# Kernel tuning notes

Hardware: AMD Instinct MI355X
Metric: run time of the kernel (lower is better)

The kernel has to match this reference:

```python
import jax, jax.numpy as jnp
import numpy as np


def lsigf_db(h, S, x, b):
    """Time-varying delayed graph filter (LSIGF_DB).
    h: (F, E, K, G) filter taps; S: (B, T, E, N, N) batch time-varying GSO;
    x: (B, T, G, N) node signals; b: (F, 1) bias or None.
    Diffusion recursion: x_k(t) = x_{k-1}(t-1) @ S(t)  (zero signal before t=0).
    """
    K = h.shape[2]
    B, T, E, N, _ = S.shape
    G = x.shape[2]
    xk = jnp.broadcast_to(x[:, :, None], (B, T, E, G, N))  # k = 0 tap
    zs = [xk]
    for _ in range(1, K):
        # delay one time step: x(t-1), zero-padded at t=0
        xk = jnp.concatenate([jnp.zeros_like(xk[:, :1]), xk[:, :-1]], axis=1)
        # shift by current GSO: matmul(x, S) as in the torch implementation
        xk = jnp.einsum('btegm,btemn->btegn', xk, S)
        zs.append(xk)
    z = jnp.stack(zs, axis=2)  # (B, T, K, E, G, N)
    y = jnp.einsum('fekg,btkegn->btfn', h, z)  # (B, T, F, N)
    if b is not None:
        y = y + b[None, None]  # (F,1) broadcasts over nodes
    return y


def setup_inputs() -> dict:
    key = jax.random.key(0)
    ks = jax.random.split(key, 12)
    B, T, E, N = 8, 64, 1, 256
    F0, F1, F2 = 12, 64, 32
    K1, K2 = 3, 3
    R1, R2 = 32, 2

    def u(k, shape, fan):
        s = 1.0 / np.sqrt(fan)
        return jax.random.uniform(k, shape, jnp.float32, -s, s)

    return {
        'x': jax.random.normal(ks[0], (B, T, F0, N), jnp.float32),
        'S': jax.random.normal(ks[1], (B, T, E, N, N), jnp.float32),
        'W1': u(ks[2], (F1, E, K1, F0), F0 * K1),
        'b1': u(ks[3], (F1, 1), F0 * K1),
        'W2': u(ks[4], (F2, E, K2, F1), F1 * K2),
        'b2': u(ks[5], (F2, 1), F1 * K2),
        'A1': u(ks[6], (R1, F2), F2),
        'c1': u(ks[7], (R1,), F2),
        'A2': u(ks[8], (R2, R1), R1),
        'c2': u(ks[9], (R2,), R1),
    }


def reference(x, S, W1, b1, W2, b2, A1, c1, A2, c2):
    # Graph filtering layers (GraphFilter_DB + Tanh)
    y = jnp.tanh(lsigf_db(W1, S, x, b1))
    y = jnp.tanh(lsigf_db(W2, S, y, b2))
    # Local readout: per-node MLP Linear -> Tanh -> Linear
    y = jnp.swapaxes(y, 2, 3)  # (B, T, N, F2)
    y = jnp.tanh(y @ A1.T + c1)
    y = y @ A2.T + c2
    return jnp.swapaxes(y, 2, 3)  # (B, T, dimReadout[-1], N)
```

## Files before the change

### kernel.cpp

```cpp
#include <hip/hip_runtime.h>
#include <hip/hip_fp16.h>

typedef _Float16 half8 __attribute__((ext_vector_type(8)));
typedef _Float16 half4v __attribute__((ext_vector_type(4)));
typedef float f32x4 __attribute__((ext_vector_type(4)));

static constexpr int B_ = 8, T_ = 64, N_ = 256;
static constexpr int F0 = 12, F1 = 64, F2 = 32;
static constexpr int BT_ = B_ * T_;

__device__ inline float tanh_fast(float x) {
    x = fminf(20.f, fmaxf(-20.f, x));
    float e = __expf(2.f * x);
    return (e - 1.f) / (e + 1.f);
}

__global__ __launch_bounds__(512) void k_transpose_s(const float* __restrict__ S,
                              _Float16* __restrict__ STh, _Float16* __restrict__ STl) {
    __shared__ float tile[64][129];
    int bt = blockIdx.x;
    int n0 = blockIdx.y * 64;
    const float* s = S + (size_t)bt * N_ * N_;
    _Float16* sth = STh + (size_t)bt * N_ * N_;
    _Float16* stl = STl + (size_t)bt * N_ * N_;
    int q = threadIdx.x & 15;
    int r0 = threadIdx.x >> 4;
    int q2 = threadIdx.x & 7;
    int nr = threadIdx.x >> 3;
    for (int m0 = 0; m0 < N_; m0 += 128) {
        #pragma unroll
        for (int rr = r0; rr < 128; rr += 32) {
            f32x4 v = __builtin_nontemporal_load(
                (const f32x4*)(s + (size_t)(m0 + rr) * N_ + n0 + q * 4));
            tile[q * 4 + 0][rr] = v[0];
            tile[q * 4 + 1][rr] = v[1];
            tile[q * 4 + 2][rr] = v[2];
            tile[q * 4 + 3][rr] = v[3];
        }
        __syncthreads();
        #pragma unroll
        for (int ci = 0; ci < 2; ++ci) {
            int mc = ci * 8 + q2;
            half8 h, l;
            #pragma unroll
            for (int e = 0; e < 8; ++e) {
                float v = tile[nr][mc * 8 + e];
                _Float16 hh = (_Float16)v;
                h[e] = hh;
                l[e] = (_Float16)(v - (float)hh);
            }
            size_t o = (size_t)(n0 + nr) * N_ + m0 + mc * 8;
            *(half8*)(sth + o) = h;
            *(half8*)(stl + o) = l;
        }
        __syncthreads();
    }
}

__global__ void k_transpose_x(const float* __restrict__ x,
                              _Float16* __restrict__ XTh, _Float16* __restrict__ XTl) {
    int bt = blockIdx.x;
    int n = threadIdx.x;
    const float* xc = x + (size_t)bt * F0 * N_;
    half8 hb[2] = {}, lb[2] = {};
    #pragma unroll
    for (int g = 0; g < F0; ++g) {
        float v = xc[(size_t)g * N_ + n];
        _Float16 hh = (_Float16)v;
        hb[g >> 3][g & 7] = hh;
        lb[g >> 3][g & 7] = (_Float16)(v - (float)hh);
    }
    size_t o = ((size_t)bt * N_ + n) * 16;
    *(half8*)(XTh + o) = hb[0];
    *(half8*)(XTh + o + 8) = hb[1];
    *(half8*)(XTl + o) = lb[0];
    *(half8*)(XTl + o + 8) = lb[1];
}

__global__ void k_chain1x(const float* __restrict__ x,
                          const _Float16* __restrict__ STh, const _Float16* __restrict__ STl,
                          _Float16* __restrict__ Oh, _Float16* __restrict__ Ol,
                          _Float16* __restrict__ OTh, _Float16* __restrict__ OTl) {
    int bt = blockIdx.x;
    int t = bt & (T_ - 1);
    int wave = threadIdx.x >> 6;
    int lane = threadIdx.x & 63;
    int l15 = lane & 15;
    int lk = lane >> 4;
    int n0 = blockIdx.y * 128 + wave * 32;

    f32x4 acc[2];
    #pragma unroll
    for (int j = 0; j < 2; ++j) acc[j] = (f32x4){0.f, 0.f, 0.f, 0.f};

    if (t > 0) {
        const float* A = x + (size_t)(bt - 1) * F0 * N_;
        const _Float16* B_h = STh + (size_t)bt * N_ * N_;
        const _Float16* B_l = STl + (size_t)bt * N_ * N_;
        #pragma unroll
        for (int kk = 0; kk < 8; ++kk) {
            int kof = kk * 32 + lk * 8;
            half8 ah = {}, al = {};
            if (l15 < F0) {
                const float* ar = A + (size_t)l15 * N_ + kof;
                float4 v0 = *(const float4*)(ar);
                float4 v1 = *(const float4*)(ar + 4);
                float vv[8] = {v0.x, v0.y, v0.z, v0.w, v1.x, v1.y, v1.z, v1.w};
                #pragma unroll
                for (int c = 0; c < 8; ++c) {
                    _Float16 hh = (_Float16)vv[c];
                    ah[c] = hh;
                    al[c] = (_Float16)(vv[c] - (float)hh);
                }
            }
            #pragma unroll
            for (int j = 0; j < 2; ++j) {
                half8 bh = *(const half8*)(B_h + (size_t)(n0 + j * 16 + l15) * N_ + kof);
                half8 bl = *(const half8*)(B_l + (size_t)(n0 + j * 16 + l15) * N_ + kof);
                acc[j] = __builtin_amdgcn_mfma_f32_16x16x32_f16(ah, bh, acc[j], 0, 0, 0);
                acc[j] = __builtin_amdgcn_mfma_f32_16x16x32_f16(al, bh, acc[j], 0, 0, 0);
                acc[j] = __builtin_amdgcn_mfma_f32_16x16x32_f16(ah, bl, acc[j], 0, 0, 0);
            }
        }
    }
    _Float16* O_h = Oh + (size_t)bt * 16 * N_;
    _Float16* O_l = Ol + (size_t)bt * 16 * N_;
    #pragma unroll
    for (int j = 0; j < 2; ++j) {
        half4v th, tl;
        #pragma unroll
        for (int r = 0; r < 4; ++r) {
            float v = acc[j][r];
            _Float16 h = (_Float16)v;
            size_t idx = (size_t)(lk * 4 + r) * N_ + n0 + j * 16 + l15;
            O_h[idx] = h;
            O_l[idx] = (_Float16)(v - (float)h);
            th[r] = h;
            tl[r] = (_Float16)(v - (float)h);
        }
        size_t to = ((size_t)bt * N_ + n0 + j * 16 + l15) * 16 + lk * 4;
        *(half4v*)(OTh + to) = th;
        *(half4v*)(OTl + to) = tl;
    }
}

__global__ void k_chainV1(const _Float16* __restrict__ Ah, const _Float16* __restrict__ Al,
                          const _Float16* __restrict__ STh, const _Float16* __restrict__ STl,
                          _Float16* __restrict__ OTh, _Float16* __restrict__ OTl) {
    int bt = blockIdx.x;
    int t = bt & (T_ - 1);
    int wave = threadIdx.x >> 6;
    int lane = threadIdx.x & 63;
    int l15 = lane & 15;
    int lk = lane >> 4;
    int n0 = blockIdx.y * 128 + wave * 32;

    f32x4 acc[2];
    #pragma unroll
    for (int j = 0; j < 2; ++j) acc[j] = (f32x4){0.f, 0.f, 0.f, 0.f};

    if (t > 0) {
        const _Float16* A_h = Ah + (size_t)(bt - 1) * 16 * N_;
        const _Float16* A_l = Al + (size_t)(bt - 1) * 16 * N_;
        const _Float16* B_h = STh + (size_t)bt * N_ * N_;
        const _Float16* B_l = STl + (size_t)bt * N_ * N_;
        #pragma unroll
        for (int kk = 0; kk < 8; ++kk) {
            int kof = kk * 32 + lk * 8;
            half8 ah = *(const half8*)(A_h + (size_t)l15 * N_ + kof);
            half8 al = *(const half8*)(A_l + (size_t)l15 * N_ + kof);
            #pragma unroll
            for (int j = 0; j < 2; ++j) {
                half8 bh = *(const half8*)(B_h + (size_t)(n0 + j * 16 + l15) * N_ + kof);
                half8 bl = *(const half8*)(B_l + (size_t)(n0 + j * 16 + l15) * N_ + kof);
                acc[j] = __builtin_amdgcn_mfma_f32_16x16x32_f16(ah, bh, acc[j], 0, 0, 0);
                acc[j] = __builtin_amdgcn_mfma_f32_16x16x32_f16(al, bh, acc[j], 0, 0, 0);
                acc[j] = __builtin_amdgcn_mfma_f32_16x16x32_f16(ah, bl, acc[j], 0, 0, 0);
            }
        }
    }
    #pragma unroll
    for (int j = 0; j < 2; ++j) {
        half4v th, tl;
        #pragma unroll
        for (int r = 0; r < 4; ++r) {
            float v = acc[j][r];
            _Float16 h = (_Float16)v;
            th[r] = h;
            tl[r] = (_Float16)(v - (float)h);
        }
        size_t to = ((size_t)bt * N_ + n0 + j * 16 + l15) * 16 + lk * 4;
        *(half4v*)(OTh + to) = th;
        *(half4v*)(OTl + to) = tl;
    }
}

__global__ void k_combine1(const _Float16* __restrict__ XTh, const _Float16* __restrict__ XTl,
                           const _Float16* __restrict__ U1Th, const _Float16* __restrict__ U1Tl,
                           const _Float16* __restrict__ V1Th, const _Float16* __restrict__ V1Tl,
                           const float* __restrict__ W1, const float* __restrict__ b1,
                           _Float16* __restrict__ Y1Th, _Float16* __restrict__ Y1Tl) {
    __shared__ _Float16 wh[64 * 72], wl[64 * 72];
    int bt = blockIdx.x;
    int tid = threadIdx.x;
    for (int i = tid; i < 64 * 72; i += 256) {
        int f = i / 72, k = i % 72;
        float v = 0.f;
        if (k < 12) v = W1[f * 36 + k];
        else if (k >= 16 && k < 28) v = W1[f * 36 + 12 + (k - 16)];
        else if (k >= 32 && k < 44) v = W1[f * 36 + 24 + (k - 32)];
        _Float16 hh = (_Float16)v;
        wh[i] = hh;
        wl[i] = (_Float16)(v - (float)hh);
    }
    __syncthreads();

    int wv = tid >> 6, lane = tid & 63, l15 = lane & 15, lk = lane >> 4;
    int n0 = wv * 64;
    f32x4 acc[4][4];
    #pragma unroll
    for (int i = 0; i < 4; ++i)
        #pragma unroll
        for (int j = 0; j < 4; ++j) acc[i][j] = (f32x4){0.f, 0.f, 0.f, 0.f};

    #pragma unroll
    for (int kk = 0; kk < 2; ++kk) {
        half8 bh[4], bl[4];
        #pragma unroll
        for (int j = 0; j < 4; ++j) {
            size_t base16 = ((size_t)bt * N_ + n0 + j * 16 + l15) * 16;
            if (kk == 0) {
                if (lk < 2) {
                    bh[j] = *(const half8*)(XTh + base16 + lk * 8);
                    bl[j] = *(const half8*)(XTl + base16 + lk * 8);
                } else {
                    bh[j] = *(const half8*)(U1Th + base16 + (lk - 2) * 8);
                    bl[j] = *(const half8*)(U1Tl + base16 + (lk - 2) * 8);
                }
            } else {
                if (lk < 2) {
                    bh[j] = *(const half8*)(V1Th + base16 + lk * 8);
                    bl[j] = *(const half8*)(V1Tl + base16 + lk * 8);
                } else {
                    bh[j] = half8{};
                    bl[j] = half8{};
                }
            }
        }
        #pragma unroll
        for (int i = 0; i < 4; ++i) {
            half8 ah = *(const half8*)(wh + (i * 16 + l15) * 72 + kk * 32 + lk * 8);
            half8 al = *(const half8*)(wl + (i * 16 + l15) * 72 + kk * 32 + lk * 8);
            #pragma unroll
            for (int j = 0; j < 4; ++j) {
                acc[i][j] = __builtin_amdgcn_mfma_f32_16x16x32_f16(ah, bh[j], acc[i][j], 0, 0, 0);
                acc[i][j] = __builtin_amdgcn_mfma_f32_16x16x32_f16(al, bh[j], acc[i][j], 0, 0, 0);
                acc[i][j] = __builtin_amdgcn_mfma_f32_16x16x32_f16(ah, bl[j], acc[i][j], 0, 0, 0);
            }
        }
    }
    #pragma unroll
    for (int i = 0; i < 4; ++i) {
        float bb[4];
        #pragma unroll
        for (int r = 0; r < 4; ++r) bb[r] = b1[i * 16 + lk * 4 + r];
        #pragma unroll
        for (int j = 0; j < 4; ++j) {
            half4v th, tl;
            #pragma unroll
            for (int r = 0; r < 4; ++r) {
                float yv = tanh_fast(acc[i][j][r] + bb[r]);
                _Float16 h = (_Float16)yv;
                th[r] = h;
                tl[r] = (_Float16)(yv - (float)h);
            }
            size_t to = ((size_t)bt * N_ + n0 + j * 16 + l15) * 64 + i * 16 + lk * 4;
            *(half4v*)(Y1Th + to) = th;
            *(half4v*)(Y1Tl + to) = tl;
        }
    }
}

__global__ void k_proj(const _Float16* __restrict__ Y1Th, const _Float16* __restrict__ Y1Tl,
                       const float* __restrict__ W2,
                       _Float16* __restrict__ Gh, _Float16* __restrict__ Gl,
                       float* __restrict__ Hf, float* __restrict__ Y2a) {
    __shared__ _Float16 wh[96 * 72], wl[96 * 72];
    int bt = blockIdx.x;
    int tid = threadIdx.x;
    for (int i = tid; i < 96 * 64; i += 256) {
        int r = i >> 6, g = i & 63;
        int f, off;
        if (r < 32)      { f = r;      off = 128; }
        else if (r < 64) { f = r - 32; off = 64;  }
        else             { f = r - 64; off = 0;   }
        float v = W2[f * 192 + off + g];
        _Float16 hh = (_Float16)v;
        wh[r * 72 + g] = hh;
        wl[r * 72 + g] = (_Float16)(v - (float)hh);
    }
    __syncthreads();

    int wv = tid >> 6, lane = tid & 63, l15 = lane & 15, lk = lane >> 4;
    int n0 = wv * 64;
    f32x4 acc[6][4];
    #pragma unroll
    for (int i = 0; i < 6; ++i)
        #pragma unroll
        for (int j = 0; j < 4; ++j) acc[i][j] = (f32x4){0.f, 0.f, 0.f, 0.f};

    const _Float16* Bh = Y1Th + (size_t)bt * N_ * 64;
    const _Float16* Bl = Y1Tl + (size_t)bt * N_ * 64;
    #pragma unroll
    for (int kk = 0; kk < 2; ++kk) {
        int kof = kk * 32 + lk * 8;
        half8 bh[4], bl[4];
        #pragma unroll
        for (int j = 0; j < 4; ++j) {
            bh[j] = *(const half8*)(Bh + (size_t)(n0 + j * 16 + l15) * 64 + kof);
            bl[j] = *(const half8*)(Bl + (size_t)(n0 + j * 16 + l15) * 64 + kof);
        }
        #pragma unroll
        for (int i = 0; i < 6; ++i) {
            half8 ah = *(const half8*)(wh + (i * 16 + l15) * 72 + kof);
            half8 al = *(const half8*)(wl + (i * 16 + l15) * 72 + kof);
            #pragma unroll
            for (int j = 0; j < 4; ++j) {
                acc[i][j] = __builtin_amdgcn_mfma_f32_16x16x32_f16(ah, bh[j], acc[i][j], 0, 0, 0);
                acc[i][j] = __builtin_amdgcn_mfma_f32_16x16x32_f16(al, bh[j], acc[i][j], 0, 0, 0);
                acc[i][j] = __builtin_amdgcn_mfma_f32_16x16x32_f16(ah, bl[j], acc[i][j], 0, 0, 0);
            }
        }
    }
    #pragma unroll
    for (int i = 0; i < 6; ++i)
        #pragma unroll
        for (int j = 0; j < 4; ++j)
            #pragma unroll
            for (int r = 0; r < 4; ++r) {
                int row = i * 16 + lk * 4 + r;
                int col = n0 + j * 16 + l15;
                float v = acc[i][j][r];
                if (row < 32) {
                    _Float16 hh = (_Float16)v;
                    size_t o = ((size_t)bt * 32 + row) * N_ + col;
                    Gh[o] = hh;
                    Gl[o] = (_Float16)(v - (float)hh);
                } else if (row < 64) {
                    Hf[((size_t)bt * 32 + row - 32) * N_ + col] = v;
                } else {
                    Y2a[((size_t)bt * 32 + row - 64) * N_ + col] = v;
                }
            }
}

__global__ void k_chainR(const _Float16* __restrict__ Gh, const _Float16* __restrict__ Gl,
                         const _Float16* __restrict__ STh, const _Float16* __restrict__ STl,
                         const float* __restrict__ Hf,
                         _Float16* __restrict__ Rh, _Float16* __restrict__ Rl) {
    int bt = blockIdx.x;
    int t = bt & (T_ - 1);
    int wave = threadIdx.x >> 6;
    int lane = threadIdx.x & 63;
    int l15 = lane & 15;
    int lk = lane >> 4;
    int n0 = blockIdx.y * 128 + wave * 32;

    f32x4 acc[2][2];
    #pragma unroll
    for (int i = 0; i < 2; ++i)
        #pragma unroll
        for (int j = 0; j < 2; ++j) acc[i][j] = (f32x4){0.f, 0.f, 0.f, 0.f};

    if (t > 0) {
        const _Float16* A_h = Gh + (size_t)(bt - 1) * 32 * N_;
        const _Float16* A_l = Gl + (size_t)(bt - 1) * 32 * N_;
        const _Float16* B_h = STh + (size_t)bt * N_ * N_;
        const _Float16* B_l = STl + (size_t)bt * N_ * N_;
        #pragma unroll
        for (int kk = 0; kk < 8; ++kk) {
            int kof = kk * 32 + lk * 8;
            half8 ah[2], al[2];
            #pragma unroll
            for (int i = 0; i < 2; ++i) {
                ah[i] = *(const half8*)(A_h + (size_t)(i * 16 + l15) * N_ + kof);
                al[i] = *(const half8*)(A_l + (size_t)(i * 16 + l15) * N_ + kof);
            }
            #pragma unroll
            for (int j = 0; j < 2; ++j) {
                half8 bh = *(const half8*)(B_h + (size_t)(n0 + j * 16 + l15) * N_ + kof);
                half8 bl = *(const half8*)(B_l + (size_t)(n0 + j * 16 + l15) * N_ + kof);
                #pragma unroll
                for (int i = 0; i < 2; ++i) {
                    acc[i][j] = __builtin_amdgcn_mfma_f32_16x16x32_f16(ah[i], bh, acc[i][j], 0, 0, 0);
                    acc[i][j] = __builtin_amdgcn_mfma_f32_16x16x32_f16(al[i], bh, acc[i][j], 0, 0, 0);
                    acc[i][j] = __builtin_amdgcn_mfma_f32_16x16x32_f16(ah[i], bl, acc[i][j], 0, 0, 0);
                }
            }
        }
    }
    const float* Hb = Hf + (size_t)bt * 32 * N_;
    _Float16* R_h = Rh + (size_t)bt * 32 * N_;
    _Float16* R_l = Rl + (size_t)bt * 32 * N_;
    #pragma unroll
    for (int i = 0; i < 2; ++i)
        #pragma unroll
        for (int j = 0; j < 2; ++j)
            #pragma unroll
            for (int r = 0; r < 4; ++r) {
                size_t idx = (size_t)(i * 16 + lk * 4 + r) * N_ + n0 + j * 16 + l15;
                float v = acc[i][j][r] + Hb[idx];
                _Float16 h = (_Float16)v;
                R_h[idx] = h;
                R_l[idx] = (_Float16)(v - (float)h);
            }
}

__global__ void k_chainY2(const _Float16* __restrict__ Rh, const _Float16* __restrict__ Rl,
                          const _Float16* __restrict__ STh, const _Float16* __restrict__ STl,
                          const float* __restrict__ Y2a, const float* __restrict__ b2,
                          const float* __restrict__ A1, const float* __restrict__ c1,
                          const float* __restrict__ A2, const float* __restrict__ c2,
                          float* __restrict__ out) {
    __shared__ float y2s[32 * 133];
    __shared__ float la1[32 * 33];
    int bt = blockIdx.x;
    int t = bt & (T_ - 1);
    int tid = threadIdx.x;
    for (int i = tid; i < 32 * 32; i += 256) la1[(i >> 5) * 33 + (i & 31)] = A1[i];

    int wave = tid >> 6;
    int lane = tid & 63;
    int l15 = lane & 15;
    int lk = lane >> 4;
    int n0 = blockIdx.y * 128 + wave * 32;

    f32x4 acc[2][2];
    #pragma unroll
    for (int i = 0; i < 2; ++i)
        #pragma unroll
        for (int j = 0; j < 2; ++j) acc[i][j] = (f32x4){0.f, 0.f, 0.f, 0.f};

    if (t > 0) {
        const _Float16* A_h = Rh + (size_t)(bt - 1) * 32 * N_;
        const _Float16* A_l = Rl + (size_t)(bt - 1) * 32 * N_;
        const _Float16* B_h = STh + (size_t)bt * N_ * N_;
        const _Float16* B_l = STl + (size_t)bt * N_ * N_;
        #pragma unroll
        for (int kk = 0; kk < 8; ++kk) {
            int kof = kk * 32 + lk * 8;
            half8 ah[2], al[2];
            #pragma unroll
            for (int i = 0; i < 2; ++i) {
                ah[i] = *(const half8*)(A_h + (size_t)(i * 16 + l15) * N_ + kof);
                al[i] = *(const half8*)(A_l + (size_t)(i * 16 + l15) * N_ + kof);
            }
            #pragma unroll
            for (int j = 0; j < 2; ++j) {
                half8 bh = *(const half8*)(B_h + (size_t)(n0 + j * 16 + l15) * N_ + kof);
                half8 bl = *(const half8*)(B_l + (size_t)(n0 + j * 16 + l15) * N_ + kof);
                #pragma unroll
                for (int i = 0; i < 2; ++i) {
                    acc[i][j] = __builtin_amdgcn_mfma_f32_16x16x32_f16(ah[i], bh, acc[i][j], 0, 0, 0);
                    acc[i][j] = __builtin_amdgcn_mfma_f32_16x16x32_f16(al[i], bh, acc[i][j], 0, 0, 0);
                    acc[i][j] = __builtin_amdgcn_mfma_f32_16x16x32_f16(ah[i], bl, acc[i][j], 0, 0, 0);
                }
            }
        }
    }
    const float* Ya = Y2a + (size_t)bt * 32 * N_;
    int colb0 = wave * 32;
    #pragma unroll
    for (int i = 0; i < 2; ++i)
        #pragma unroll
        for (int j = 0; j < 2; ++j)
            #pragma unroll
            for (int r = 0; r < 4; ++r) {
                int row = i * 16 + lk * 4 + r;
                int colb = colb0 + j * 16 + l15;
                int n = blockIdx.y * 128 + colb;
                y2s[row * 133 + colb] = acc[i][j][r] + Ya[(size_t)row * N_ + n] + b2[row];
            }
    __syncthreads();

    if (tid < 128) {
        int colb = tid;
        int n = blockIdx.y * 128 + colb;
        float y2v[32];
        #pragma unroll
        for (int f = 0; f < 32; ++f) y2v[f] = tanh_fast(y2s[f * 133 + colb]);
        float o0 = 0.f, o1 = 0.f;
        #pragma unroll
        for (int j = 0; j < 32; ++j) {
            const float* a1r = la1 + j * 33;
            float s = c1[j];
            #pragma unroll
            for (int f = 0; f < 32; ++f) s += a1r[f] * y2v[f];
            float hj = tanh_fast(s);
            o0 += A2[j] * hj;
            o1 += A2[32 + j] * hj;
        }
        out[((size_t)bt * 2 + 0) * N_ + n] = o0 + c2[0];
        out[((size_t)bt * 2 + 1) * N_ + n] = o1 + c2[1];
    }
}

extern "C" void kernel_launch(void* const* d_in, const int* in_sizes, int n_in,
                              void* d_out, int out_size, void* d_ws, size_t ws_size,
                              hipStream_t stream) {
    const float* x  = (const float*)d_in[0];
    const float* S  = (const float*)d_in[1];
    const float* W1 = (const float*)d_in[2];
    const float* b1 = (const float*)d_in[3];
    const float* W2 = (const float*)d_in[4];
    const float* b2 = (const float*)d_in[5];
    const float* A1 = (const float*)d_in[6];
    const float* c1 = (const float*)d_in[7];
    const float* A2 = (const float*)d_in[8];
    const float* c2 = (const float*)d_in[9];
    float* out = (float*)d_out;

    char* ws = (char*)d_ws;
    const size_t SZ_ST  = (size_t)BT_ * N_ * N_ * 2;
    const size_t SZ_Y1T = (size_t)BT_ * N_ * 64 * 2;
    const size_t SZ_G   = (size_t)BT_ * 32 * N_ * 2;
    const size_t SZ_H   = (size_t)BT_ * 32 * N_ * 4;
    const size_t SZ_T16 = (size_t)BT_ * N_ * 16 * 2;
    size_t off = 0;
    _Float16* STh  = (_Float16*)(ws + off); off += SZ_ST;
    _Float16* STl  = (_Float16*)(ws + off); off += SZ_ST;
    _Float16* Y1Th = (_Float16*)(ws + off); off += SZ_Y1T;
    _Float16* Y1Tl = (_Float16*)(ws + off); off += SZ_Y1T;
    _Float16* Gh   = (_Float16*)(ws + off); off += SZ_G;
    _Float16* Gl   = (_Float16*)(ws + off); off += SZ_G;
    float*    Hf   = (float*)(ws + off); off += SZ_H;
    float*    Y2a  = (float*)(ws + off); off += SZ_H;
    _Float16* Rh   = (_Float16*)(ws + off); off += SZ_G;
    _Float16* Rl   = (_Float16*)(ws + off); off += SZ_G;
    if (ws_size < off) return;

    _Float16* XTh  = (_Float16*)Hf;
    _Float16* XTl  = XTh + SZ_T16 / 2;
    _Float16* U1Th = (_Float16*)Y2a;
    _Float16* U1Tl = U1Th + SZ_T16 / 2;
    _Float16* V1Th = U1Tl + SZ_T16 / 2;
    _Float16* V1Tl = V1Th + SZ_T16 / 2;
    _Float16* U1h  = Rh;
    _Float16* U1l  = Rl;

    k_transpose_s<<<dim3(BT_, 4), 512, 0, stream>>>(S, STh, STl);
    k_transpose_x<<<BT_, 256, 0, stream>>>(x, XTh, XTl);
    k_chain1x<<<dim3(BT_, 2), 256, 0, stream>>>(x, STh, STl, U1h, U1l, U1Th, U1Tl);
    k_chainV1<<<dim3(BT_, 2), 256, 0, stream>>>(U1h, U1l, STh, STl, V1Th, V1Tl);
    k_combine1<<<BT_, 256, 0, stream>>>(XTh, XTl, U1Th, U1Tl, V1Th, V1Tl, W1, b1, Y1Th, Y1Tl);
    k_proj<<<BT_, 256, 0, stream>>>(Y1Th, Y1Tl, W2, Gh, Gl, Hf, Y2a);
    k_chainR<<<dim3(BT_, 2), 256, 0, stream>>>(Gh, Gl, STh, STl, Hf, Rh, Rl);
    k_chainY2<<<dim3(BT_, 2), 256, 0, stream>>>(Rh, Rl, STh, STl, Y2a, b2,
                                                A1, c1, A2, c2, out);
}
```

Measured before the change: 247.4 us.

## Fuse first diffusion step into S transpose kernel using shared-memory tile

The S transpose/split kernel now also computes the first diffusion product x(t-1)·S(t), taking the B operand straight from the fp32 shared-memory tile instead of rereading the fp16 hi/lo copies from global memory in a separate kernel. This removes one launch and one full pass over STh/STl. Block size drops from 512 to 256 threads, so each thread loads and converts twice as many elements. The MFMA work is now spread over the transpose grid's 4 column blocks.

```diff
diff --git a/kernel.cpp b/kernel.cpp
--- a/kernel.cpp
+++ b/kernel.cpp
@@ -15,21 +15,29 @@
     return (e - 1.f) / (e + 1.f);
 }
 
-__global__ __launch_bounds__(512) void k_transpose_s(const float* __restrict__ S,
-                              _Float16* __restrict__ STh, _Float16* __restrict__ STl) {
+__global__ __launch_bounds__(256) void k_transpose_u1(
+    const float* __restrict__ S, const float* __restrict__ x,
+    _Float16* __restrict__ STh, _Float16* __restrict__ STl,
+    _Float16* __restrict__ U1h, _Float16* __restrict__ U1l,
+    _Float16* __restrict__ U1Th, _Float16* __restrict__ U1Tl) {
     __shared__ float tile[64][129];
     int bt = blockIdx.x;
+    int t  = bt & (T_ - 1);
     int n0 = blockIdx.y * 64;
     const float* s = S + (size_t)bt * N_ * N_;
     _Float16* sth = STh + (size_t)bt * N_ * N_;
     _Float16* stl = STl + (size_t)bt * N_ * N_;
-    int q = threadIdx.x & 15;
-    int r0 = threadIdx.x >> 4;
-    int q2 = threadIdx.x & 7;
-    int nr = threadIdx.x >> 3;
+    int tid = threadIdx.x;
+    int q  = tid & 15, r0  = tid >> 4;
+    int q2 = tid & 7,  nr0 = tid >> 3;
+    int lane = tid & 63, wv = tid >> 6;
+    int l15 = lane & 15, lk = lane >> 4;
+    const float* A = x + (size_t)(bt - 1) * F0 * N_;
+    f32x4 acc = (f32x4){0.f, 0.f, 0.f, 0.f};
+
     for (int m0 = 0; m0 < N_; m0 += 128) {
         #pragma unroll
-        for (int rr = r0; rr < 128; rr += 32) {
+        for (int rr = r0; rr < 128; rr += 16) {
             f32x4 v = __builtin_nontemporal_load(
                 (const f32x4*)(s + (size_t)(m0 + rr) * N_ + n0 + q * 4));
             tile[q * 4 + 0][rr] = v[0];
@@ -39,21 +47,74 @@
         }
         __syncthreads();
         #pragma unroll
-        for (int ci = 0; ci < 2; ++ci) {
-            int mc = ci * 8 + q2;
-            half8 h, l;
-            #pragma unroll
-            for (int e = 0; e < 8; ++e) {
-                float v = tile[nr][mc * 8 + e];
-                _Float16 hh = (_Float16)v;
-                h[e] = hh;
-                l[e] = (_Float16)(v - (float)hh);
-            }
-            size_t o = (size_t)(n0 + nr) * N_ + m0 + mc * 8;
-            *(half8*)(sth + o) = h;
-            *(half8*)(stl + o) = l;
+        for (int nn = nr0; nn < 64; nn += 32) {
+            #pragma unroll
+            for (int ci = 0; ci < 2; ++ci) {
+                int mc = ci * 8 + q2;
+                half8 h, l;
+                #pragma unroll
+                for (int e = 0; e < 8; ++e) {
+                    float v = tile[nn][mc * 8 + e];
+                    _Float16 hh = (_Float16)v;
+                    h[e] = hh;
+                    l[e] = (_Float16)(v - (float)hh);
+                }
+                size_t o = (size_t)(n0 + nn) * N_ + m0 + mc * 8;
+                *(half8*)(sth + o) = h;
+                *(half8*)(stl + o) = l;
+            }
+        }
+        if (t > 0) {
+            #pragma unroll
+            for (int kkl = 0; kkl < 4; ++kkl) {
+                int ml = kkl * 32 + lk * 8;
+                half8 ah = {}, al = {};
+                if (l15 < F0) {
+                    const float* ar = A + (size_t)l15 * N_ + m0 + ml;
+                    float4 v0 = *(const float4*)(ar);
+                    float4 v1 = *(const float4*)(ar + 4);
+                    float vv[8] = {v0.x, v0.y, v0.z, v0.w, v1.x, v1.y, v1.z, v1.w};
+                    #pragma unroll
+                    for (int c = 0; c < 8; ++c) {
+                        _Float16 hh = (_Float16)vv[c];
+                        ah[c] = hh;
+                        al[c] = (_Float16)(vv[c] - (float)hh);
+                    }
+                }
+                half8 bh, bl;
+                const float* tr = &tile[wv * 16 + l15][ml];
+                #pragma unroll
+                for (int e = 0; e < 8; ++e) {
+                    float v = tr[e];
+                    _Float16 hh = (_Float16)v;
+                    bh[e] = hh;
+                    bl[e] = (_Float16)(v - (float)hh);
+                }
+                acc = __builtin_amdgcn_mfma_f32_16x16x32_f16(ah, bh, acc, 0, 0, 0);
+                acc = __builtin_amdgcn_mfma_f32_16x16x32_f16(al, bh, acc, 0, 0, 0);
+                acc = __builtin_amdgcn_mfma_f32_16x16x32_f16(ah, bl, acc, 0, 0, 0);
+            }
         }
         __syncthreads();
+    }
+    {
+        int n = n0 + wv * 16 + l15;
+        _Float16* O_h = U1h + (size_t)bt * 16 * N_;
+        _Float16* O_l = U1l + (size_t)bt * 16 * N_;
+        half4v th, tl;
+        #pragma unroll
+        for (int r = 0; r < 4; ++r) {
+            float v = acc[r];
+            _Float16 h = (_Float16)v;
+            _Float16 lo = (_Float16)(v - (float)h);
+            O_h[(size_t)(lk * 4 + r) * N_ + n] = h;
+            O_l[(size_t)(lk * 4 + r) * N_ + n] = lo;
+            th[r] = h;
+            tl[r] = lo;
+        }
+        size_t to = ((size_t)bt * N_ + n) * 16 + lk * 4;
+        *(half4v*)(U1Th + to) = th;
+        *(half4v*)(U1Tl + to) = tl;
     }
 }
 
@@ -75,73 +136,6 @@
     *(half8*)(XTh + o + 8) = hb[1];
     *(half8*)(XTl + o) = lb[0];
     *(half8*)(XTl + o + 8) = lb[1];
-}
-
-__global__ void k_chain1x(const float* __restrict__ x,
-                          const _Float16* __restrict__ STh, const _Float16* __restrict__ STl,
-                          _Float16* __restrict__ Oh, _Float16* __restrict__ Ol,
-                          _Float16* __restrict__ OTh, _Float16* __restrict__ OTl) {
-    int bt = blockIdx.x;
-    int t = bt & (T_ - 1);
-    int wave = threadIdx.x >> 6;
-    int lane = threadIdx.x & 63;
-    int l15 = lane & 15;
-    int lk = lane >> 4;
-    int n0 = blockIdx.y * 128 + wave * 32;
-
-    f32x4 acc[2];
-    #pragma unroll
-    for (int j = 0; j < 2; ++j) acc[j] = (f32x4){0.f, 0.f, 0.f, 0.f};
-
-    if (t > 0) {
-        const float* A = x + (size_t)(bt - 1) * F0 * N_;
-        const _Float16* B_h = STh + (size_t)bt * N_ * N_;
-        const _Float16* B_l = STl + (size_t)bt * N_ * N_;
-        #pragma unroll
-        for (int kk = 0; kk < 8; ++kk) {
-            int kof = kk * 32 + lk * 8;
-            half8 ah = {}, al = {};
-            if (l15 < F0) {
-                const float* ar = A + (size_t)l15 * N_ + kof;
-                float4 v0 = *(const float4*)(ar);
-                float4 v1 = *(const float4*)(ar + 4);
-                float vv[8] = {v0.x, v0.y, v0.z, v0.w, v1.x, v1.y, v1.z, v1.w};
-                #pragma unroll
-                for (int c = 0; c < 8; ++c) {
-                    _Float16 hh = (_Float16)vv[c];
-                    ah[c] = hh;
-                    al[c] = (_Float16)(vv[c] - (float)hh);
-                }
-            }
-            #pragma unroll
-            for (int j = 0; j < 2; ++j) {
-                half8 bh = *(const half8*)(B_h + (size_t)(n0 + j * 16 + l15) * N_ + kof);
-                half8 bl = *(const half8*)(B_l + (size_t)(n0 + j * 16 + l15) * N_ + kof);
-                acc[j] = __builtin_amdgcn_mfma_f32_16x16x32_f16(ah, bh, acc[j], 0, 0, 0);
-                acc[j] = __builtin_amdgcn_mfma_f32_16x16x32_f16(al, bh, acc[j], 0, 0, 0);
-                acc[j] = __builtin_amdgcn_mfma_f32_16x16x32_f16(ah, bl, acc[j], 0, 0, 0);
-            }
-        }
-    }
-    _Float16* O_h = Oh + (size_t)bt * 16 * N_;
-    _Float16* O_l = Ol + (size_t)bt * 16 * N_;
-    #pragma unroll
-    for (int j = 0; j < 2; ++j) {
-        half4v th, tl;
-        #pragma unroll
-        for (int r = 0; r < 4; ++r) {
-            float v = acc[j][r];
-            _Float16 h = (_Float16)v;
-            size_t idx = (size_t)(lk * 4 + r) * N_ + n0 + j * 16 + l15;
-            O_h[idx] = h;
-            O_l[idx] = (_Float16)(v - (float)h);
-            th[r] = h;
-            tl[r] = (_Float16)(v - (float)h);
-        }
-        size_t to = ((size_t)bt * N_ + n0 + j * 16 + l15) * 16 + lk * 4;
-        *(half4v*)(OTh + to) = th;
-        *(half4v*)(OTl + to) = tl;
-    }
 }
 
 __global__ void k_chainV1(const _Float16* __restrict__ Ah, const _Float16* __restrict__ Al,
@@ -548,9 +542,9 @@
     _Float16* U1h  = Rh;
     _Float16* U1l  = Rl;
 
-    k_transpose_s<<<dim3(BT_, 4), 512, 0, stream>>>(S, STh, STl);
+    k_transpose_u1<<<dim3(BT_, 4), 256, 0, stream>>>(S, x, STh, STl,
+                                                     U1h, U1l, U1Th, U1Tl);
     k_transpose_x<<<BT_, 256, 0, stream>>>(x, XTh, XTl);
-    k_chain1x<<<dim3(BT_, 2), 256, 0, stream>>>(x, STh, STl, U1h, U1l, U1Th, U1Tl);
     k_chainV1<<<dim3(BT_, 2), 256, 0, stream>>>(U1h, U1l, STh, STl, V1Th, V1Tl);
     k_combine1<<<BT_, 256, 0, stream>>>(XTh, XTl, U1Th, U1Tl, V1Th, V1Tl, W1, b1, Y1Th, Y1Tl);
     k_proj<<<BT_, 256, 0, stream>>>(Y1Th, Y1Tl, W2, Gh, Gl, Hf, Y2a);
```

Measured after the change: 228.9 us. 1.08x faster.
